# Kernel optimization log

Measured on AMD Instinct MI355X. Metric: run time of the kernel, lower is better.

## Reference

```python
import jax, jax.numpy as jnp
import numpy as np

N_NODES = 50000
N_EDGES = 800000
IN_DIM, HID, OUT_DIM = 128, 64, 64


def setup_inputs() -> dict:
    key = jax.random.key(0)
    ks = jax.random.split(key, 12)
    inp = {
        "x": jax.random.normal(ks[0], (N_NODES, IN_DIM), dtype=jnp.float32),
        "edge_index": jax.random.randint(ks[1], (2, N_EDGES), 0, N_NODES, dtype=jnp.int32),
    }
    dims = [(IN_DIM, HID), (HID, HID), (HID, HID), (HID, HID), (HID, OUT_DIM)]
    for i, (di, do) in enumerate(dims, start=1):
        scale = (2.0 / (di + do)) ** 0.5  # glorot-like
        inp[f"W{i}"] = jax.random.normal(ks[1 + i], (di, do), dtype=jnp.float32) * scale
        inp[f"b{i}"] = jnp.zeros((do,), dtype=jnp.float32)
    return inp


def _edge_norm(edge_index, n_nodes):
    # GCNConv(improved=True): add self-loops with weight 2.0, symmetric norm.
    src, dst = edge_index[0], edge_index[1]
    loop = jnp.arange(n_nodes, dtype=edge_index.dtype)
    src_f = jnp.concatenate([src, loop])
    dst_f = jnp.concatenate([dst, loop])
    w = jnp.concatenate([
        jnp.ones((src.shape[0],), jnp.float32),
        jnp.full((n_nodes,), 2.0, jnp.float32),
    ])
    deg = jax.ops.segment_sum(w, dst_f, num_segments=n_nodes)
    dinv = jnp.where(deg > 0, jax.lax.rsqrt(deg), 0.0)
    norm = dinv[src_f] * w * dinv[dst_f]  # [E+N]
    return src_f, dst_f, norm


def reference(x, edge_index, W1, b1, W2, b2, W3, b3, W4, b4, W5, b5):
    n = x.shape[0]
    src_f, dst_f, norm = _edge_norm(edge_index, n)

    def conv(h, W, b):
        h = h @ W                                  # [N, d_out]
        msg = h[src_f] * norm[:, None]             # gather + edge normalize
        return jax.ops.segment_sum(msg, dst_f, num_segments=n) + b

    h = jax.nn.relu(conv(x, W1, b1))
    h = jax.nn.relu(conv(h, W2, b2))
    h = jax.nn.relu(conv(h, W3, b3))
    h = jax.nn.relu(conv(h, W4, b4))
    return conv(h, W5, b5)
```

## Files before the change

### kernel.cpp

```cpp
#include <hip/hip_runtime.h>

#define NN 50000
#define NE 800000

__device__ __forceinline__ float bf2f(unsigned short u) {
    union { unsigned int i; float f; } v; v.i = ((unsigned int)u) << 16; return v.f;
}
__device__ __forceinline__ unsigned short f2bf(float f) {
    union { float f; unsigned int i; } v; v.f = f;
    unsigned int r = v.i + 0x7fffu + ((v.i >> 16) & 1u);
    return (unsigned short)(r >> 16);
}
__device__ __forceinline__ float rdlane_f(float x, int l) {
    return __uint_as_float(__builtin_amdgcn_readlane(__float_as_uint(x), l));
}

__global__ void k_zero(float4* __restrict__ p, int n16) {
    int i = blockIdx.x * 256 + threadIdx.x;
    if (i < n16) p[i] = make_float4(0.f, 0.f, 0.f, 0.f);
}


__global__ void k_count(const int* __restrict__ dst, int* __restrict__ cnt, int E) {
    int e = blockIdx.x * 256 + threadIdx.x;
    if (e < E) atomicAdd(&cnt[dst[e]], 1);
}

__global__ void k_dinv(const int* __restrict__ cnt, float* __restrict__ dinv, int N) {
    int i = blockIdx.x * 256 + threadIdx.x;
    if (i < N) dinv[i] = rsqrtf(2.0f + (float)cnt[i]);
}

__global__ void k_scanA(const int* __restrict__ cnt, int* __restrict__ row_ptr,
                        int* __restrict__ bsum, int N) {
    __shared__ int buf[256];
    int i = blockIdx.x * 256 + threadIdx.x;
    int v = (i < N) ? cnt[i] : 0;
    buf[threadIdx.x] = v;
    __syncthreads();
    for (int off = 1; off < 256; off <<= 1) {
        int t = (threadIdx.x >= off) ? buf[threadIdx.x - off] : 0;
        __syncthreads();
        buf[threadIdx.x] += t;
        __syncthreads();
    }
    if (i < N) row_ptr[i] = buf[threadIdx.x] - v;
    if (threadIdx.x == 255) bsum[blockIdx.x] = buf[255];
}

__global__ void k_scanB(int* __restrict__ bsum, int nb) {
    __shared__ int buf[256];
    int v = (threadIdx.x < nb) ? bsum[threadIdx.x] : 0;
    buf[threadIdx.x] = v;
    __syncthreads();
    for (int off = 1; off < 256; off <<= 1) {
        int t = (threadIdx.x >= off) ? buf[threadIdx.x - off] : 0;
        __syncthreads();
        buf[threadIdx.x] += t;
        __syncthreads();
    }
    if (threadIdx.x < nb) bsum[threadIdx.x] = buf[threadIdx.x] - v;
}

__global__ void k_scanC(int* __restrict__ row_ptr, const int* __restrict__ bsum,
                        int N, int E) {
    int i = blockIdx.x * 256 + threadIdx.x;
    if (i < N) row_ptr[i] += bsum[blockIdx.x];
    if (i == 0) row_ptr[N] = E;
}

__global__ void k_fill(const int* __restrict__ src, const int* __restrict__ dst,
                       const float* __restrict__ dinv, const int* __restrict__ row_ptr,
                       int* __restrict__ cursor, int2* __restrict__ csr, int E) {
    int e = blockIdx.x * 256 + threadIdx.x;
    if (e >= E) return;
    int s = src[e], d = dst[e];
    int pos = row_ptr[d] + atomicAdd(&cursor[d], 1);
    float nm = dinv[s] * dinv[d];
    csr[pos] = make_int2(s, __float_as_int(nm));
}


__global__ __launch_bounds__(256, 4) void k_gemm128(const float* __restrict__ X,
                                                    const float* __restrict__ W,
                                                    unsigned short* __restrict__ H, int N) {
    const int K = 128;
    __shared__ float Ws[K * 64];
    for (int i = threadIdx.x; i < K * 16; i += 256)
        ((float4*)Ws)[i] = ((const float4*)W)[i];
    __syncthreads();

    const int g  = threadIdx.x >> 3;
    const int c0 = (threadIdx.x & 7) * 8;
    const int r0 = blockIdx.x * 64 + g * 2;
    const int r1 = r0 + 1;
    const bool v0 = r0 < N, v1 = r1 < N;

    float a00=0,a01=0,a02=0,a03=0,a04=0,a05=0,a06=0,a07=0;
    float a10=0,a11=0,a12=0,a13=0,a14=0,a15=0,a16=0,a17=0;

    const float* x0 = X + (size_t)r0 * K;
    const float* x1 = X + (size_t)r1 * K;

#pragma unroll 1
    for (int k0 = 0; k0 < K; k0 += 4) {
        float4 xa = v0 ? *(const float4*)(x0 + k0) : make_float4(0, 0, 0, 0);
        float4 xb = v1 ? *(const float4*)(x1 + k0) : make_float4(0, 0, 0, 0);
#pragma unroll
        for (int kk = 0; kk < 4; ++kk) {
            const float xs0 = (kk == 0) ? xa.x : (kk == 1) ? xa.y : (kk == 2) ? xa.z : xa.w;
            const float xs1 = (kk == 0) ? xb.x : (kk == 1) ? xb.y : (kk == 2) ? xb.z : xb.w;
            const float* wr = &Ws[(k0 + kk) * 64 + c0];
            const float4 w0 = *(const float4*)(wr);
            const float4 w1 = *(const float4*)(wr + 4);
            a00 = fmaf(xs0, w0.x, a00); a01 = fmaf(xs0, w0.y, a01);
            a02 = fmaf(xs0, w0.z, a02); a03 = fmaf(xs0, w0.w, a03);
            a04 = fmaf(xs0, w1.x, a04); a05 = fmaf(xs0, w1.y, a05);
            a06 = fmaf(xs0, w1.z, a06); a07 = fmaf(xs0, w1.w, a07);
            a10 = fmaf(xs1, w0.x, a10); a11 = fmaf(xs1, w0.y, a11);
            a12 = fmaf(xs1, w0.z, a12); a13 = fmaf(xs1, w0.w, a13);
            a14 = fmaf(xs1, w1.x, a14); a15 = fmaf(xs1, w1.y, a15);
            a16 = fmaf(xs1, w1.z, a16); a17 = fmaf(xs1, w1.w, a17);
        }
    }

    if (v0) {
        uint4 p;
        p.x = (unsigned)f2bf(a00) | ((unsigned)f2bf(a01) << 16);
        p.y = (unsigned)f2bf(a02) | ((unsigned)f2bf(a03) << 16);
        p.z = (unsigned)f2bf(a04) | ((unsigned)f2bf(a05) << 16);
        p.w = (unsigned)f2bf(a06) | ((unsigned)f2bf(a07) << 16);
        *(uint4*)&H[(size_t)r0 * 64 + c0] = p;
    }
    if (v1) {
        uint4 p;
        p.x = (unsigned)f2bf(a10) | ((unsigned)f2bf(a11) << 16);
        p.y = (unsigned)f2bf(a12) | ((unsigned)f2bf(a13) << 16);
        p.z = (unsigned)f2bf(a14) | ((unsigned)f2bf(a15) << 16);
        p.w = (unsigned)f2bf(a16) | ((unsigned)f2bf(a17) << 16);
        *(uint4*)&H[(size_t)r1 * 64 + c0] = p;
    }
}


template <bool RELU>
__device__ __forceinline__ void agg_row2(const unsigned short* __restrict__ H,
                                         const long long* __restrict__ csr_ll,
                                         const float4& b4, float di0, float di1,
                                         int i0, int i1, int s0, int e0, int s1, int e1,
                                         int lane, int g, int c4,
                                         float4& r0, float4& r1) {
    ushort4 hs0 = *(const ushort4*)&H[(size_t)i0 * 64 + c4];
    ushort4 hs1 = *(const ushort4*)&H[(size_t)i1 * 64 + c4];

    int ee0 = s0 + lane, ee1 = s1 + lane;
    long long pk0 = (ee0 < e0) ? csr_ll[ee0] : 0LL;
    long long pk1 = (ee1 < e1) ? csr_ll[ee1] : 0LL;
    int px0 = (int)pk0, py0 = (int)(pk0 >> 32);
    int px1 = (int)pk1, py1 = (int)(pk1 >> 32);

    int m0 = e0 - s0; if (m0 > 64) m0 = 64;
    int m1 = e1 - s1; if (m1 > 64) m1 = 64;
    int nt0 = (m0 + 3) >> 2, nt1 = (m1 + 3) >> 2;
    int ntm = nt0 > nt1 ? nt0 : nt1;

    float4 acc0 = make_float4(0.f, 0.f, 0.f, 0.f);
    float4 acc1 = make_float4(0.f, 0.f, 0.f, 0.f);

#pragma unroll 4
    for (int t = 0; t < ntm; ++t) {
        int sl = t * 4 + g;
        if (t < nt0) {
            int ss   = __shfl(px0, sl);
            float nn = __uint_as_float(__shfl(py0, sl));
            ushort4 h = *(const ushort4*)&H[(size_t)ss * 64 + c4];
            acc0.x = fmaf(bf2f(h.x), nn, acc0.x);
            acc0.y = fmaf(bf2f(h.y), nn, acc0.y);
            acc0.z = fmaf(bf2f(h.z), nn, acc0.z);
            acc0.w = fmaf(bf2f(h.w), nn, acc0.w);
        }
        if (t < nt1) {
            int ss   = __shfl(px1, sl);
            float nn = __uint_as_float(__shfl(py1, sl));
            ushort4 h = *(const ushort4*)&H[(size_t)ss * 64 + c4];
            acc1.x = fmaf(bf2f(h.x), nn, acc1.x);
            acc1.y = fmaf(bf2f(h.y), nn, acc1.y);
            acc1.z = fmaf(bf2f(h.z), nn, acc1.z);
            acc1.w = fmaf(bf2f(h.w), nn, acc1.w);
        }
    }

    for (int base = s0 + 64; base < e0; base += 64) {
        int e = base + lane;
        long long pk = (e < e0) ? csr_ll[e] : 0LL;
        int px = (int)pk, py = (int)(pk >> 32);
        int m = e0 - base; if (m > 64) m = 64;
        int nt = (m + 3) >> 2;
        for (int t = 0; t < nt; ++t) {
            int sl = t * 4 + g;
            int ss = __shfl(px, sl);
            float nn = __uint_as_float(__shfl(py, sl));
            ushort4 h = *(const ushort4*)&H[(size_t)ss * 64 + c4];
            acc0.x = fmaf(bf2f(h.x), nn, acc0.x);
            acc0.y = fmaf(bf2f(h.y), nn, acc0.y);
            acc0.z = fmaf(bf2f(h.z), nn, acc0.z);
            acc0.w = fmaf(bf2f(h.w), nn, acc0.w);
        }
    }
    for (int base = s1 + 64; base < e1; base += 64) {
        int e = base + lane;
        long long pk = (e < e1) ? csr_ll[e] : 0LL;
        int px = (int)pk, py = (int)(pk >> 32);
        int m = e1 - base; if (m > 64) m = 64;
        int nt = (m + 3) >> 2;
        for (int t = 0; t < nt; ++t) {
            int sl = t * 4 + g;
            int ss = __shfl(px, sl);
            float nn = __uint_as_float(__shfl(py, sl));
            ushort4 h = *(const ushort4*)&H[(size_t)ss * 64 + c4];
            acc1.x = fmaf(bf2f(h.x), nn, acc1.x);
            acc1.y = fmaf(bf2f(h.y), nn, acc1.y);
            acc1.z = fmaf(bf2f(h.z), nn, acc1.z);
            acc1.w = fmaf(bf2f(h.w), nn, acc1.w);
        }
    }

#pragma unroll
    for (int d = 16; d <= 32; d <<= 1) {
        acc0.x += __shfl_xor(acc0.x, d); acc0.y += __shfl_xor(acc0.y, d);
        acc0.z += __shfl_xor(acc0.z, d); acc0.w += __shfl_xor(acc0.w, d);
        acc1.x += __shfl_xor(acc1.x, d); acc1.y += __shfl_xor(acc1.y, d);
        acc1.z += __shfl_xor(acc1.z, d); acc1.w += __shfl_xor(acc1.w, d);
    }

    float sa = 2.0f * di0 * di0, sb = 2.0f * di1 * di1;
    r0.x = acc0.x + sa * bf2f(hs0.x) + b4.x;
    r0.y = acc0.y + sa * bf2f(hs0.y) + b4.y;
    r0.z = acc0.z + sa * bf2f(hs0.z) + b4.z;
    r0.w = acc0.w + sa * bf2f(hs0.w) + b4.w;
    r1.x = acc1.x + sb * bf2f(hs1.x) + b4.x;
    r1.y = acc1.y + sb * bf2f(hs1.y) + b4.y;
    r1.z = acc1.z + sb * bf2f(hs1.z) + b4.z;
    r1.w = acc1.w + sb * bf2f(hs1.w) + b4.w;
    if (RELU) {
        r0.x = fmaxf(r0.x, 0.f); r0.y = fmaxf(r0.y, 0.f);
        r0.z = fmaxf(r0.z, 0.f); r0.w = fmaxf(r0.w, 0.f);
        r1.x = fmaxf(r1.x, 0.f); r1.y = fmaxf(r1.y, 0.f);
        r1.z = fmaxf(r1.z, 0.f); r1.w = fmaxf(r1.w, 0.f);
    }
}

__global__ __launch_bounds__(256, 8) void k_fused(const unsigned short* __restrict__ H,
                                                  const int* __restrict__ row_ptr,
                                                  const long long* __restrict__ csr_ll,
                                                  const float* __restrict__ dinv,
                                                  const float* __restrict__ bias,
                                                  const float* __restrict__ Wn,
                                                  unsigned short* __restrict__ Hout, int N) {
    const int wid  = threadIdx.x >> 6;
    const int lane = threadIdx.x & 63;
    const int i0   = (blockIdx.x * 4 + wid) * 2;
    const int i1   = i0 + 1;
    const int g    = lane >> 4;
    const int c4   = (lane & 15) * 4;

    int idx = i0 + lane;
    int   rp = (lane <= 2) ? row_ptr[idx] : 0;
    float dv = (lane <  2) ? dinv[idx]    : 0.f;

    const float4 b4 = *(const float4*)&bias[c4];
    int s0 = __shfl(rp, 0), sm = __shfl(rp, 1), e1 = __shfl(rp, 2);
    float di0 = __shfl(dv, 0), di1 = __shfl(dv, 1);

    float4 r0, r1;
    agg_row2<true>(H, csr_ll, b4, di0, di1, i0, i1, s0, sm, sm, e1,
                   lane, g, c4, r0, r1);

    float y0 = 0.f, y1 = 0.f;
#pragma unroll
    for (int q = 0; q < 16; ++q) {
        float w0 = Wn[(4 * q + 0) * 64 + lane];
        float w1 = Wn[(4 * q + 1) * 64 + lane];
        float w2 = Wn[(4 * q + 2) * 64 + lane];
        float w3 = Wn[(4 * q + 3) * 64 + lane];
        y0 = fmaf(rdlane_f(r0.x, q), w0, y0);
        y0 = fmaf(rdlane_f(r0.y, q), w1, y0);
        y0 = fmaf(rdlane_f(r0.z, q), w2, y0);
        y0 = fmaf(rdlane_f(r0.w, q), w3, y0);
        y1 = fmaf(rdlane_f(r1.x, q), w0, y1);
        y1 = fmaf(rdlane_f(r1.y, q), w1, y1);
        y1 = fmaf(rdlane_f(r1.z, q), w2, y1);
        y1 = fmaf(rdlane_f(r1.w, q), w3, y1);
    }
    Hout[(size_t)i0 * 64 + lane] = f2bf(y0);
    Hout[(size_t)i1 * 64 + lane] = f2bf(y1);
}

__global__ __launch_bounds__(256, 8) void k_agg_last(const unsigned short* __restrict__ H,
                                                     const int* __restrict__ row_ptr,
                                                     const long long* __restrict__ csr_ll,
                                                     const float* __restrict__ dinv,
                                                     const float* __restrict__ bias,
                                                     float* __restrict__ out, int N) {
    const int wid  = threadIdx.x >> 6;
    const int lane = threadIdx.x & 63;
    const int i0   = (blockIdx.x * 4 + wid) * 2;
    const int i1   = i0 + 1;
    const int g    = lane >> 4;
    const int c4   = (lane & 15) * 4;

    const float4 b4 = *(const float4*)&bias[c4];

    int idx = i0 + lane;
    int   rp = (lane <= 2) ? row_ptr[idx] : 0;
    float dv = (lane <  2) ? dinv[idx]    : 0.f;
    int s0 = __shfl(rp, 0), sm = __shfl(rp, 1), e1 = __shfl(rp, 2);
    float di0 = __shfl(dv, 0), di1 = __shfl(dv, 1);

    float4 r0, r1;
    agg_row2<false>(H, csr_ll, b4, di0, di1, i0, i1, s0, sm, sm, e1,
                    lane, g, c4, r0, r1);
    if (g == 0) {
        *(float4*)&out[(size_t)i0 * 64 + c4] = r0;
        *(float4*)&out[(size_t)i1 * 64 + c4] = r1;
    }
}


extern "C" void kernel_launch(void* const* d_in, const int* in_sizes, int n_in,
                              void* d_out, int out_size, void* d_ws, size_t ws_size,
                              hipStream_t stream) {
    (void)in_sizes; (void)n_in; (void)out_size; (void)ws_size;

    const float* x  = (const float*)d_in[0];
    const int*   ei = (const int*)d_in[1];
    const float* Wl[5] = {(const float*)d_in[2], (const float*)d_in[4], (const float*)d_in[6],
                          (const float*)d_in[8], (const float*)d_in[10]};
    const float* bl[5] = {(const float*)d_in[3], (const float*)d_in[5], (const float*)d_in[7],
                          (const float*)d_in[9], (const float*)d_in[11]};
    float* out = (float*)d_out;

    const int* src = ei;
    const int* dst = ei + NE;

    char* ws = (char*)d_ws;
    size_t off = 0;
    auto alloc = [&](size_t bytes) -> void* {
        void* p = ws + off;
        off += (bytes + 255) & ~(size_t)255;
        return p;
    };
    int*   cnt      = (int*)alloc(NN * 4);
    int*   cursor   = (int*)alloc(NN * 4);
    size_t zero_bytes = (size_t)((char*)(cursor + NN) - (char*)cnt);
    int*   row_ptr  = (int*)alloc((NN + 1) * 4);
    int*   bsum     = (int*)alloc(256 * 4);
    float* dinv     = (float*)alloc(NN * 4);
    int2*  csr      = (int2*)alloc((size_t)NE * 8);
    unsigned short* Hb  = (unsigned short*)alloc((size_t)NN * 64 * 2);
    unsigned short* Hb2 = (unsigned short*)alloc((size_t)NN * 64 * 2);

    int n16 = (int)((zero_bytes + 15) / 16);
    k_zero<<<(n16 + 255) / 256, 256, 0, stream>>>((float4*)cnt, n16);

    int ebl = (NE + 255) / 256;
    int nbl = (NN + 255) / 256;
    k_count<<<ebl, 256, 0, stream>>>(dst, cnt, NE);
    k_dinv<<<nbl, 256, 0, stream>>>(cnt, dinv, NN);
    k_scanA<<<nbl, 256, 0, stream>>>(cnt, row_ptr, bsum, NN);
    k_scanB<<<1, 256, 0, stream>>>(bsum, nbl);
    k_scanC<<<nbl, 256, 0, stream>>>(row_ptr, bsum, NN, NE);
    k_fill<<<ebl, 256, 0, stream>>>(src, dst, dinv, row_ptr, cursor, csr, NE);

    const long long* csr_ll = (const long long*)csr;
    int gg = (NN + 63) / 64;
    int ga = NN / 8;

    k_gemm128<<<gg, 256, 0, stream>>>(x, Wl[0], Hb, NN);
    k_fused<<<ga, 256, 0, stream>>>(Hb,  row_ptr, csr_ll, dinv, bl[0], Wl[1], Hb2, NN);
    k_fused<<<ga, 256, 0, stream>>>(Hb2, row_ptr, csr_ll, dinv, bl[1], Wl[2], Hb,  NN);
    k_fused<<<ga, 256, 0, stream>>>(Hb,  row_ptr, csr_ll, dinv, bl[2], Wl[3], Hb2, NN);
    k_fused<<<ga, 256, 0, stream>>>(Hb2, row_ptr, csr_ll, dinv, bl[3], Wl[4], Hb,  NN);
    k_agg_last<<<ga, 256, 0, stream>>>(Hb, row_ptr, csr_ll, dinv, bl[4], out, NN);
}
```

Baseline: 273.8 us.

## Pack CSR entries into 32 bits and fuse CSR fill with first GEMM

Each CSR entry now holds a 16-bit source index and an fp16 edge norm in one 32-bit word instead of an int2, halving index traffic in every aggregation layer. The CSR fill kernel and the first 128-wide GEMM are merged into one launch with disjoint block ranges so they can overlap. This relies on the node count fitting in 16 bits and reduces the precision of edge weights to fp16.

```diff
diff --git a/kernel.cpp b/kernel.cpp
--- a/kernel.cpp
+++ b/kernel.cpp
@@ -1,7 +1,9 @@
 #include <hip/hip_runtime.h>
+#include <hip/hip_fp16.h>
 
 #define NN 50000
 #define NE 800000
+#define FILLB ((NE + 255) / 256)
 
 __device__ __forceinline__ float bf2f(unsigned short u) {
     union { unsigned int i; float f; } v; v.i = ((unsigned int)u) << 16; return v.f;
@@ -10,9 +12,6 @@
     union { float f; unsigned int i; } v; v.f = f;
     unsigned int r = v.i + 0x7fffu + ((v.i >> 16) & 1u);
     return (unsigned short)(r >> 16);
-}
-__device__ __forceinline__ float rdlane_f(float x, int l) {
-    return __uint_as_float(__builtin_amdgcn_readlane(__float_as_uint(x), l));
 }
 
 __global__ void k_zero(float4* __restrict__ p, int n16) {
@@ -69,30 +68,35 @@
     if (i == 0) row_ptr[N] = E;
 }
 
-__global__ void k_fill(const int* __restrict__ src, const int* __restrict__ dst,
-                       const float* __restrict__ dinv, const int* __restrict__ row_ptr,
-                       int* __restrict__ cursor, int2* __restrict__ csr, int E) {
-    int e = blockIdx.x * 256 + threadIdx.x;
-    if (e >= E) return;
-    int s = src[e], d = dst[e];
-    int pos = row_ptr[d] + atomicAdd(&cursor[d], 1);
-    float nm = dinv[s] * dinv[d];
-    csr[pos] = make_int2(s, __float_as_int(nm));
-}
-
-
-__global__ __launch_bounds__(256, 4) void k_gemm128(const float* __restrict__ X,
-                                                    const float* __restrict__ W,
-                                                    unsigned short* __restrict__ H, int N) {
+
+__global__ __launch_bounds__(256, 4) void k_fill_gemm(
+        const int* __restrict__ src, const int* __restrict__ dst,
+        const float* __restrict__ dinv, const int* __restrict__ row_ptr,
+        int* __restrict__ cursor, unsigned* __restrict__ csr,
+        const float* __restrict__ X, const float* __restrict__ W,
+        unsigned short* __restrict__ H, int N) {
+    __shared__ float Ws[128 * 64];
+
+    if (blockIdx.x < FILLB) {
+        int e = blockIdx.x * 256 + threadIdx.x;
+        if (e >= NE) return;
+        int s = src[e], d = dst[e];
+        int pos = row_ptr[d] + atomicAdd(&cursor[d], 1);
+        float nm = dinv[s] * dinv[d];
+        csr[pos] = (unsigned)s |
+                   ((unsigned)__half_as_ushort(__float2half(nm)) << 16);
+        return;
+    }
+
     const int K = 128;
-    __shared__ float Ws[K * 64];
+    const int bid = blockIdx.x - FILLB;
     for (int i = threadIdx.x; i < K * 16; i += 256)
         ((float4*)Ws)[i] = ((const float4*)W)[i];
     __syncthreads();
 
     const int g  = threadIdx.x >> 3;
     const int c0 = (threadIdx.x & 7) * 8;
-    const int r0 = blockIdx.x * 64 + g * 2;
+    const int r0 = bid * 64 + g * 2;
     const int r1 = r0 + 1;
     const bool v0 = r0 < N, v1 = r1 < N;
 
@@ -143,9 +147,14 @@
 }
 
 
+__device__ __forceinline__ void unpack(unsigned w, int& ss, float& nn) {
+    ss = (int)(w & 0xffffu);
+    nn = __half2float(__ushort_as_half((unsigned short)(w >> 16)));
+}
+
 template <bool RELU>
 __device__ __forceinline__ void agg_row2(const unsigned short* __restrict__ H,
-                                         const long long* __restrict__ csr_ll,
+                                         const unsigned* __restrict__ csr,
                                          const float4& b4, float di0, float di1,
                                          int i0, int i1, int s0, int e0, int s1, int e1,
                                          int lane, int g, int c4,
@@ -154,10 +163,8 @@
     ushort4 hs1 = *(const ushort4*)&H[(size_t)i1 * 64 + c4];
 
     int ee0 = s0 + lane, ee1 = s1 + lane;
-    long long pk0 = (ee0 < e0) ? csr_ll[ee0] : 0LL;
-    long long pk1 = (ee1 < e1) ? csr_ll[ee1] : 0LL;
-    int px0 = (int)pk0, py0 = (int)(pk0 >> 32);
-    int px1 = (int)pk1, py1 = (int)(pk1 >> 32);
+    unsigned pk0 = (ee0 < e0) ? csr[ee0] : 0u;
+    unsigned pk1 = (ee1 < e1) ? csr[ee1] : 0u;
 
     int m0 = e0 - s0; if (m0 > 64) m0 = 64;
     int m1 = e1 - s1; if (m1 > 64) m1 = 64;
@@ -171,8 +178,8 @@
     for (int t = 0; t < ntm; ++t) {
         int sl = t * 4 + g;
         if (t < nt0) {
-            int ss   = __shfl(px0, sl);
-            float nn = __uint_as_float(__shfl(py0, sl));
+            unsigned w = __shfl(pk0, sl);
+            int ss; float nn; unpack(w, ss, nn);
             ushort4 h = *(const ushort4*)&H[(size_t)ss * 64 + c4];
             acc0.x = fmaf(bf2f(h.x), nn, acc0.x);
             acc0.y = fmaf(bf2f(h.y), nn, acc0.y);
@@ -180,8 +187,8 @@
             acc0.w = fmaf(bf2f(h.w), nn, acc0.w);
         }
         if (t < nt1) {
-            int ss   = __shfl(px1, sl);
-            float nn = __uint_as_float(__shfl(py1, sl));
+            unsigned w = __shfl(pk1, sl);
+            int ss; float nn; unpack(w, ss, nn);
             ushort4 h = *(const ushort4*)&H[(size_t)ss * 64 + c4];
             acc1.x = fmaf(bf2f(h.x), nn, acc1.x);
             acc1.y = fmaf(bf2f(h.y), nn, acc1.y);
@@ -192,14 +199,12 @@
 
     for (int base = s0 + 64; base < e0; base += 64) {
         int e = base + lane;
-        long long pk = (e < e0) ? csr_ll[e] : 0LL;
-        int px = (int)pk, py = (int)(pk >> 32);
+        unsigned pk = (e < e0) ? csr[e] : 0u;
         int m = e0 - base; if (m > 64) m = 64;
         int nt = (m + 3) >> 2;
         for (int t = 0; t < nt; ++t) {
-            int sl = t * 4 + g;
-            int ss = __shfl(px, sl);
-            float nn = __uint_as_float(__shfl(py, sl));
+            unsigned w = __shfl(pk, t * 4 + g);
+            int ss; float nn; unpack(w, ss, nn);
             ushort4 h = *(const ushort4*)&H[(size_t)ss * 64 + c4];
             acc0.x = fmaf(bf2f(h.x), nn, acc0.x);
             acc0.y = fmaf(bf2f(h.y), nn, acc0.y);
@@ -209,14 +214,12 @@
     }
     for (int base = s1 + 64; base < e1; base += 64) {
         int e = base + lane;
-        long long pk = (e < e1) ? csr_ll[e] : 0LL;
-        int px = (int)pk, py = (int)(pk >> 32);
+        unsigned pk = (e < e1) ? csr[e] : 0u;
         int m = e1 - base; if (m > 64) m = 64;
         int nt = (m + 3) >> 2;
         for (int t = 0; t < nt; ++t) {
-            int sl = t * 4 + g;
-            int ss = __shfl(px, sl);
-            float nn = __uint_as_float(__shfl(py, sl));
+            unsigned w = __shfl(pk, t * 4 + g);
+            int ss; float nn; unpack(w, ss, nn);
             ushort4 h = *(const ushort4*)&H[(size_t)ss * 64 + c4];
             acc1.x = fmaf(bf2f(h.x), nn, acc1.x);
             acc1.y = fmaf(bf2f(h.y), nn, acc1.y);
@@ -250,9 +253,13 @@
     }
 }
 
+__device__ __forceinline__ float rdlane_f(float x, int l) {
+    return __uint_as_float(__builtin_amdgcn_readlane(__float_as_uint(x), l));
+}
+
 __global__ __launch_bounds__(256, 8) void k_fused(const unsigned short* __restrict__ H,
                                                   const int* __restrict__ row_ptr,
-                                                  const long long* __restrict__ csr_ll,
+                                                  const unsigned* __restrict__ csr,
                                                   const float* __restrict__ dinv,
                                                   const float* __restrict__ bias,
                                                   const float* __restrict__ Wn,
@@ -273,7 +280,7 @@
     float di0 = __shfl(dv, 0), di1 = __shfl(dv, 1);
 
     float4 r0, r1;
-    agg_row2<true>(H, csr_ll, b4, di0, di1, i0, i1, s0, sm, sm, e1,
+    agg_row2<true>(H, csr, b4, di0, di1, i0, i1, s0, sm, sm, e1,
                    lane, g, c4, r0, r1);
 
     float y0 = 0.f, y1 = 0.f;
@@ -298,7 +305,7 @@
 
 __global__ __launch_bounds__(256, 8) void k_agg_last(const unsigned short* __restrict__ H,
                                                      const int* __restrict__ row_ptr,
-                                                     const long long* __restrict__ csr_ll,
+                                                     const unsigned* __restrict__ csr,
                                                      const float* __restrict__ dinv,
                                                      const float* __restrict__ bias,
                                                      float* __restrict__ out, int N) {
@@ -318,7 +325,7 @@
     float di0 = __shfl(dv, 0), di1 = __shfl(dv, 1);
 
     float4 r0, r1;
-    agg_row2<false>(H, csr_ll, b4, di0, di1, i0, i1, s0, sm, sm, e1,
+    agg_row2<false>(H, csr, b4, di0, di1, i0, i1, s0, sm, sm, e1,
                     lane, g, c4, r0, r1);
     if (g == 0) {
         *(float4*)&out[(size_t)i0 * 64 + c4] = r0;
@@ -350,13 +357,13 @@
         off += (bytes + 255) & ~(size_t)255;
         return p;
     };
-    int*   cnt      = (int*)alloc(NN * 4);
-    int*   cursor   = (int*)alloc(NN * 4);
+    int*      cnt     = (int*)alloc(NN * 4);
+    int*      cursor  = (int*)alloc(NN * 4);
     size_t zero_bytes = (size_t)((char*)(cursor + NN) - (char*)cnt);
-    int*   row_ptr  = (int*)alloc((NN + 1) * 4);
-    int*   bsum     = (int*)alloc(256 * 4);
-    float* dinv     = (float*)alloc(NN * 4);
-    int2*  csr      = (int2*)alloc((size_t)NE * 8);
+    int*      row_ptr = (int*)alloc((NN + 1) * 4);
+    int*      bsum    = (int*)alloc(256 * 4);
+    float*    dinv    = (float*)alloc(NN * 4);
+    unsigned* csr     = (unsigned*)alloc((size_t)NE * 4);
     unsigned short* Hb  = (unsigned short*)alloc((size_t)NN * 64 * 2);
     unsigned short* Hb2 = (unsigned short*)alloc((size_t)NN * 64 * 2);
 
@@ -365,21 +372,20 @@
 
     int ebl = (NE + 255) / 256;
     int nbl = (NN + 255) / 256;
+    int gg  = (NN + 63) / 64;
     k_count<<<ebl, 256, 0, stream>>>(dst, cnt, NE);
     k_dinv<<<nbl, 256, 0, stream>>>(cnt, dinv, NN);
     k_scanA<<<nbl, 256, 0, stream>>>(cnt, row_ptr, bsum, NN);
     k_scanB<<<1, 256, 0, stream>>>(bsum, nbl);
     k_scanC<<<nbl, 256, 0, stream>>>(row_ptr, bsum, NN, NE);
-    k_fill<<<ebl, 256, 0, stream>>>(src, dst, dinv, row_ptr, cursor, csr, NE);
-
-    const long long* csr_ll = (const long long*)csr;
-    int gg = (NN + 63) / 64;
+    k_fill_gemm<<<FILLB + gg, 256, 0, stream>>>(src, dst, dinv, row_ptr, cursor,
+                                                csr, x, Wl[0], Hb, NN);
+
     int ga = NN / 8;
 
-    k_gemm128<<<gg, 256, 0, stream>>>(x, Wl[0], Hb, NN);
-    k_fused<<<ga, 256, 0, stream>>>(Hb,  row_ptr, csr_ll, dinv, bl[0], Wl[1], Hb2, NN);
-    k_fused<<<ga, 256, 0, stream>>>(Hb2, row_ptr, csr_ll, dinv, bl[1], Wl[2], Hb,  NN);
-    k_fused<<<ga, 256, 0, stream>>>(Hb,  row_ptr, csr_ll, dinv, bl[2], Wl[3], Hb2, NN);
-    k_fused<<<ga, 256, 0, stream>>>(Hb2, row_ptr, csr_ll, dinv, bl[3], Wl[4], Hb,  NN);
-    k_agg_last<<<ga, 256, 0, stream>>>(Hb, row_ptr, csr_ll, dinv, bl[4], out, NN);
-}
+    k_fused<<<ga, 256, 0, stream>>>(Hb,  row_ptr, csr, dinv, bl[0], Wl[1], Hb2, NN);
+    k_fused<<<ga, 256, 0, stream>>>(Hb2, row_ptr, csr, dinv, bl[1], Wl[2], Hb,  NN);
+    k_fused<<<ga, 256, 0, stream>>>(Hb,  row_ptr, csr, dinv, bl[2], Wl[3], Hb2, NN);
+    k_fused<<<ga, 256, 0, stream>>>(Hb2, row_ptr, csr, dinv, bl[3], Wl[4], Hb,  NN);
+    k_agg_last<<<ga, 256, 0, stream>>>(Hb, row_ptr, csr, dinv, bl[4], out, NN);
+}
```

New measurement: 266.9 us. -2.5%, faster.
